# Kernel optimization log

Measured on AMD Instinct MI355X. Metric: run time of the kernel, lower is better.

Reference implementation:

```python
import jax, jax.numpy as jnp
import numpy as np

N_NODES = 50000
N_EDGES = 300000
HID = 256


def setup_inputs() -> dict:
    key = jax.random.key(0)
    ks = jax.random.split(key, 8)
    s = lambda fan_in: 1.0 / np.sqrt(fan_in)
    return {
        "node_embeddings": jax.random.normal(ks[0], (N_NODES, HID), dtype=jnp.float32),
        "edge_index": jax.random.randint(ks[1], (2, N_EDGES), 0, N_NODES, dtype=jnp.int64),
        "edge_attr": jax.random.normal(ks[2], (N_EDGES, 3), dtype=jnp.float32),
        "W1": jax.random.normal(ks[3], (2 * HID + 3, HID), dtype=jnp.float32) * s(2 * HID + 3),
        "b1": jnp.zeros((HID,), dtype=jnp.float32),
        "W2": jax.random.normal(ks[4], (HID, HID // 2), dtype=jnp.float32) * s(HID),
        "b2": jnp.zeros((HID // 2,), dtype=jnp.float32),
        "W3": jax.random.normal(ks[5], (HID // 2, HID // 4), dtype=jnp.float32) * s(HID // 2),
        "b3": jnp.zeros((HID // 4,), dtype=jnp.float32),
        "W4": jax.random.normal(ks[6], (HID // 4, 3), dtype=jnp.float32) * s(HID // 4),
        "b4": jnp.zeros((3,), dtype=jnp.float32),
    }


def reference(node_embeddings, edge_index, edge_attr, W1, b1, W2, b2, W3, b3, W4, b4):
    # Gather source/target node embeddings: [E, H] each
    src = node_embeddings[edge_index[0]]
    dst = node_embeddings[edge_index[1]]
    feats = jnp.concatenate([src, dst, edge_attr], axis=-1)  # [E, 2H+3]
    # edge_encoder: Linear -> ReLU -> (Dropout=identity in eval) -> Linear
    h = jax.nn.relu(feats @ W1 + b1)
    h = h @ W2 + b2  # [E, H//2]
    # classifier: Linear -> ReLU -> Linear
    h = jax.nn.relu(h @ W3 + b3)
    logits = h @ W4 + b4  # [E, 3]
    return logits
```

## Files before the change

kernel.cpp:

```cpp
#include <hip/hip_runtime.h>
#include <hip/hip_bf16.h>
#include <stdint.h>
#include <stddef.h>


#define NN 50000
#define NE 300000
#define KG(kq,g2) ((kq)*2+(g2))

using bf16x8 = __attribute__((ext_vector_type(8))) short;
using f32x16 = __attribute__((ext_vector_type(16))) float;
using f32x4  = __attribute__((ext_vector_type(4))) float;
using f32x2  = __attribute__((ext_vector_type(2))) float;
using u32x4  = __attribute__((ext_vector_type(4))) unsigned int;
using u32x2  = __attribute__((ext_vector_type(2))) unsigned int;

#define OFF_PQ   0ULL
#define SZ_PQ    (50000ULL*512ULL*2ULL)
#define OFF_W1   (OFF_PQ + SZ_PQ)
#define SZ_W1    (512ULL*256ULL*2ULL)
#define OFF_W1C  (OFF_W1 + SZ_W1)
#define SZ_W1C   (3ULL*256ULL*4ULL)
#define OFF_W2   (OFF_W1C + SZ_W1C)
#define SZ_W2    (128ULL*256ULL*2ULL)
#define OFF_W3   (OFF_W2 + SZ_W2)
#define SZ_W3    (64ULL*128ULL*2ULL)
#define OFF_W4   (OFF_W3 + SZ_W3)
#define SZ_W4    (16ULL*64ULL*2ULL)
#define OFF_FLAG (OFF_W4 + SZ_W4)
#define WS_NEED  (OFF_FLAG + 16ULL)

__device__ __forceinline__ unsigned short f2bf(float x){
  unsigned u = __float_as_uint(x);
  unsigned r = 0x7FFFu + ((u >> 16) & 1u);
  return (unsigned short)((u + r) >> 16);
}
__device__ __forceinline__ unsigned cvtpk(float lo, float hi){
  unsigned r;
  asm("v_cvt_pk_bf16_f32 %0, %1, %2" : "=v"(r) : "v"(lo), "v"(hi));
  return r;
}
__device__ __forceinline__ f32x2 unpk(unsigned w){
  f32x2 r;
  r[0] = __uint_as_float(w << 16);
  r[1] = __uint_as_float(w & 0xFFFF0000u);
  return r;
}
__device__ __forceinline__ f32x16 mfma32(bf16x8 a, bf16x8 b, f32x16 c){
  return __builtin_amdgcn_mfma_f32_32x32x16_bf16(a, b, c, 0, 0, 0);
}
__device__ __forceinline__ f32x4 mfma16(bf16x8 a, bf16x8 b, f32x4 c){
  return __builtin_amdgcn_mfma_f32_16x16x32_bf16(a, b, c, 0, 0, 0);
}
__device__ __forceinline__ f32x16 zero16(){
  f32x16 v;
#pragma unroll
  for (int i = 0; i < 16; ++i) v[i] = 0.f;
  return v;
}

__global__ void prep_pack(const float* __restrict__ W1, const float* __restrict__ W2,
                          const float* __restrict__ W3, const float* __restrict__ W4,
                          const int* __restrict__ ei32, char* __restrict__ ws)
{
  int i = blockIdx.x * 256 + threadIdx.x;
  unsigned short* w1i = (unsigned short*)(ws + OFF_W1);
  unsigned short* w2i = (unsigned short*)(ws + OFF_W2);
  unsigned short* w3i = (unsigned short*)(ws + OFF_W3);
  unsigned short* w4i = (unsigned short*)(ws + OFF_W4);

  if (i < 131072){
    int j = i & 7, out = (i >> 3) & 511, kg = i >> 12;
    int k = (kg >> 1)*16 + (kg & 1)*8 + j;
    float v = (out < 256) ? W1[(size_t)k*256 + out]
                          : W1[(size_t)(256 + k)*256 + (out - 256)];
    w1i[i] = f2bf(v);
  } else if (i < 131072 + 32768){
    int i2 = i - 131072;
    int j = i2 & 7, out = (i2 >> 3) & 127, sg = i2 >> 10;
    int k = (sg >> 2)*32 + (sg & 3)*8 + j;
    w2i[i2] = f2bf(W2[(size_t)k*128 + out]);
  } else if (i < 131072 + 32768 + 8192){
    int i3 = i - 131072 - 32768;
    int j = i3 & 7, out = (i3 >> 3) & 63, sg = i3 >> 9;
    int k = (sg >> 2)*32 + (sg & 3)*8 + j;
    w3i[i3] = f2bf(W3[(size_t)k*64 + out]);
  } else if (i < 131072 + 32768 + 8192 + 1024){
    int i4 = i - 131072 - 32768 - 8192;
    int j = i4 & 7, out = (i4 >> 3) & 15, sg = i4 >> 7;
    int k = (sg >> 2)*32 + (sg & 3)*8 + j;
    w4i[i4] = (out < 3) ? f2bf(W4[(size_t)k*3 + out]) : (unsigned short)0;
  }
  if (i < 768){
    float* w1c = (float*)(ws + OFF_W1C);
    w1c[i] = W1[(size_t)(512 + i/256)*256 + (i & 255)];
  }
  if (i == 0){
    int f = 1;
    for (int t = 1; t < 64; t += 2) if (ei32[t] != 0) { f = 0; break; }
    *(int*)(ws + OFF_FLAG) = f;
  }
}

__global__ __launch_bounds__(512, 4) void gemm1(const float* __restrict__ emb,
                                                const float* __restrict__ b1,
                                                char* __restrict__ ws)
{
  __shared__ __align__(16) unsigned short embL[32*64*8];

  const int tid = threadIdx.x;
  const int wv = tid >> 6, l = tid & 63, ln = l & 31, g2 = l >> 5;
  const int bid = blockIdx.x;
  const int nb = (bid >> 1) * 64;
  const int oh = bid & 1;
  const int ob = oh*256 + wv*32;
  const unsigned short* w1L = (const unsigned short*)(ws + OFF_W1);
  unsigned short* PQ = (unsigned short*)(ws + OFF_PQ);

  bf16x8 aw[16];
#pragma unroll
  for (int kq = 0; kq < 16; ++kq)
    aw[kq] = *(const bf16x8*)(w1L + ((size_t)KG(kq,g2)*512 + ob + ln)*8);

#pragma unroll
  for (int it = 0; it < 8; ++it){
    int u = it*512 + tid;
    int kg = u >> 7, node = (u >> 1) & 63, half = u & 1;
    int n = nb + node; if (n >= NN) n = NN - 1;
    int k = (kg >> 1)*16 + (kg & 1)*8 + half*4;
    f32x4 e = *(const f32x4*)(emb + (size_t)n*256 + k);
    u32x2 w; w[0] = cvtpk(e[0], e[1]); w[1] = cvtpk(e[2], e[3]);
    *(u32x2*)(embL + (size_t)kg*512 + node*8 + half*4) = w;
  }
  __syncthreads();

  f32x16 acc0 = zero16(), acc1 = zero16();
#pragma unroll
  for (int kq = 0; kq < 16; ++kq){
    bf16x8 b0  = *(const bf16x8*)(embL + ((size_t)KG(kq,g2)*64 +      ln)*8);
    bf16x8 b1v = *(const bf16x8*)(embL + ((size_t)KG(kq,g2)*64 + 32 + ln)*8);
    acc0 = mfma32(aw[kq], b0,  acc0);
    acc1 = mfma32(aw[kq], b1v, acc1);
  }

#pragma unroll
  for (int bg = 0; bg < 2; ++bg){
    int n = nb + bg*32 + ln;
    if (n < NN){
#pragma unroll
      for (int rr = 0; rr < 4; ++rr){
        int o = ob + rr*8 + g2*4;
        f32x4 bv = {0.f,0.f,0.f,0.f};
        if (oh == 0) bv = *(const f32x4*)(b1 + o);
        unsigned d0, d1;
        if (bg == 0){
          d0 = cvtpk(acc0[rr*4+0]+bv[0], acc0[rr*4+1]+bv[1]);
          d1 = cvtpk(acc0[rr*4+2]+bv[2], acc0[rr*4+3]+bv[3]);
        } else {
          d0 = cvtpk(acc1[rr*4+0]+bv[0], acc1[rr*4+1]+bv[1]);
          d1 = cvtpk(acc1[rr*4+2]+bv[2], acc1[rr*4+3]+bv[3]);
        }
        u32x2 st = {d0, d1};
        *(u32x2*)(PQ + (size_t)n*512 + o) = st;
      }
    }
  }
}


#define PAIRX(LO, HI, D) ((D)==0 ? (f32x2){(LO)[0],(LO)[1]} : \
                          (D)==1 ? (f32x2){(LO)[2],(LO)[3]} : \
                          (D)==2 ? (f32x2){(HI)[0],(HI)[1]} : \
                                   (f32x2){(HI)[2],(HI)[3]})

#define L2STEP(S, PC, QC)                                                      \
  {                                                                            \
    const int ks_ = (S);                                                       \
    const int kb = ks_*32 + g4*8;                                              \
    f32x4 w0lo = *(const f32x4*)(w1c_lds +   0 + kb);                          \
    f32x4 w0hi = *(const f32x4*)(w1c_lds +   4 + kb);                          \
    f32x4 w1lo = *(const f32x4*)(w1c_lds + 256 + kb);                          \
    f32x4 w1hi = *(const f32x4*)(w1c_lds + 260 + kb);                          \
    f32x4 w2lo = *(const f32x4*)(w1c_lds + 512 + kb);                          \
    f32x4 w2hi = *(const f32x4*)(w1c_lds + 516 + kb);                          \
    u32x4 pu = __builtin_bit_cast(u32x4, PC);                                  \
    u32x4 qu = __builtin_bit_cast(u32x4, QC);                                  \
    f32x2 z2 = {0.f, 0.f};                                                     \
    unsigned bu0, bu1, bu2, bu3;                                               \
    _Pragma("unroll")                                                          \
    for (int d = 0; d < 4; ++d){                                               \
      f32x2 h = unpk(pu[d]) + unpk(qu[d]);                                     \
      h += PAIRX(w0lo, w0hi, d) * at0;                                         \
      h += PAIRX(w1lo, w1hi, d) * at1;                                         \
      h += PAIRX(w2lo, w2hi, d) * at2;                                         \
      h = __builtin_elementwise_max(h, z2);                                    \
      unsigned c = cvtpk(h[0], h[1]);                                          \
      if (d==0) bu0 = c; else if (d==1) bu1 = c; else if (d==2) bu2 = c;       \
      else bu3 = c;                                                            \
    }                                                                          \
    u32x4 buv = {bu0, bu1, bu2, bu3};                                          \
    bf16x8 b = __builtin_bit_cast(bf16x8, buv);                                \
    const char* abase = smem + (size_t)(ks_*4 + g4)*2048 + c16*16;             \
    _Pragma("unroll")                                                          \
    for (int t = 0; t < 8; ++t){                                               \
      bf16x8 af = *(const bf16x8*)(abase + t*256);                             \
      acc2[t] = mfma16(af, b, acc2[t]);                                        \
    }                                                                          \
  }

__global__ __launch_bounds__(512, 4) void fused(const int* __restrict__ eidx,
                                                const float* __restrict__ attr,
                                                const float* __restrict__ b2,
                                                const float* __restrict__ b3,
                                                const float* __restrict__ b4,
                                                const char* __restrict__ ws,
                                                float* __restrict__ out)
{
  __shared__ __align__(16) char smem[68608];
  const int tid = threadIdx.x;
  const int wv = tid >> 6, l = tid & 63, c16 = l & 15, g4 = l >> 4;

  const unsigned short* PQ = (const unsigned short*)(ws + OFF_PQ);
  const float* W1c = (const float*)(ws + OFF_W1C);
  const int flag64 = *(const int*)(ws + OFF_FLAG);
  const float* w1c_lds = (const float*)(smem + 65536);

  const int eb = blockIdx.x * 128 + wv * 16;
  const int e = eb + c16;
  const bool ev = (e < NE);
  const int ec = ev ? e : 0;
  const int si = flag64 ? eidx[2*(size_t)ec]        : eidx[ec];
  const int di = flag64 ? eidx[2*((size_t)NE + ec)] : eidx[NE + ec];

  const unsigned short* Prow = PQ + (size_t)si*512 + g4*8;
  const unsigned short* Qrow = PQ + (size_t)di*512 + 256 + g4*8;
  bf16x8 p0 = *(const bf16x8*)(Prow +   0), p1 = *(const bf16x8*)(Prow +  32);
  bf16x8 p2 = *(const bf16x8*)(Prow +  64), p3 = *(const bf16x8*)(Prow +  96);
  bf16x8 p4 = *(const bf16x8*)(Prow + 128), p5 = *(const bf16x8*)(Prow + 160);
  bf16x8 p6 = *(const bf16x8*)(Prow + 192), p7 = *(const bf16x8*)(Prow + 224);
  bf16x8 q0 = *(const bf16x8*)(Qrow +   0), q1 = *(const bf16x8*)(Qrow +  32);
  bf16x8 q2 = *(const bf16x8*)(Qrow +  64), q3 = *(const bf16x8*)(Qrow +  96);
  bf16x8 q4 = *(const bf16x8*)(Qrow + 128), q5 = *(const bf16x8*)(Qrow + 160);
  bf16x8 q6 = *(const bf16x8*)(Qrow + 192), q7 = *(const bf16x8*)(Qrow + 224);

  const float at0 = ev ? attr[(size_t)ec*3 + 0] : 0.f;
  const float at1 = ev ? attr[(size_t)ec*3 + 1] : 0.f;
  const float at2 = ev ? attr[(size_t)ec*3 + 2] : 0.f;

  {
    const uint4* src = (const uint4*)(ws + OFF_W2);
    uint4* dst = (uint4*)smem;
#pragma unroll
    for (int it = 0; it < 8; ++it) dst[it*512 + tid] = src[it*512 + tid];
    if (tid < 192) ((f32x4*)(smem + 65536))[tid] = ((const f32x4*)W1c)[tid];
  }
  __syncthreads();

  f32x4 acc2[8];
#pragma unroll
  for (int t = 0; t < 8; ++t) acc2[t] = (f32x4){0.f,0.f,0.f,0.f};

  L2STEP(0, p0, q0);
  L2STEP(1, p1, q1);
  L2STEP(2, p2, q2);
  L2STEP(3, p3, q3);
  L2STEP(4, p4, q4);
  L2STEP(5, p5, q5);
  L2STEP(6, p6, q6);
  L2STEP(7, p7, q7);

  __syncthreads();

  {
    const uint4* s3 = (const uint4*)(ws + OFF_W3);
    uint4* d3 = (uint4*)(smem + 36864);
    for (int i = tid; i < 1152; i += 512) d3[i] = s3[i];
  }

  unsigned short* hslot = (unsigned short*)(smem + wv*4352);
#pragma unroll
  for (int t = 0; t < 8; ++t){
    f32x4 bv = *(const f32x4*)(b2 + t*16 + g4*4);
    unsigned d0 = cvtpk(acc2[t][0]+bv[0], acc2[t][1]+bv[1]);
    unsigned d1 = cvtpk(acc2[t][2]+bv[2], acc2[t][3]+bv[3]);
    u32x2 st = {d0, d1};
    *(u32x2*)(hslot + (size_t)c16*136 + t*16 + g4*4) = st;
  }
  __syncthreads();

  f32x4 acc3[4];
#pragma unroll
  for (int t = 0; t < 4; ++t) acc3[t] = (f32x4){0.f,0.f,0.f,0.f};
  const char* w3b = smem + 36864;
#pragma unroll
  for (int ks = 0; ks < 4; ++ks){
    bf16x8 bb = *(const bf16x8*)(hslot + (size_t)c16*136 + ks*32 + g4*8);
    const char* ab = w3b + (size_t)(ks*4 + g4)*1024 + c16*16;
#pragma unroll
    for (int t = 0; t < 4; ++t){
      bf16x8 af = *(const bf16x8*)(ab + t*256);
      acc3[t] = mfma16(af, bb, acc3[t]);
    }
  }

#pragma unroll
  for (int t = 0; t < 4; ++t){
    f32x4 bv = *(const f32x4*)(b3 + t*16 + g4*4);
    unsigned d0 = cvtpk(fmaxf(acc3[t][0]+bv[0],0.f), fmaxf(acc3[t][1]+bv[1],0.f));
    unsigned d1 = cvtpk(fmaxf(acc3[t][2]+bv[2],0.f), fmaxf(acc3[t][3]+bv[3],0.f));
    u32x2 st = {d0, d1};
    *(u32x2*)(hslot + (size_t)c16*136 + t*16 + g4*4) = st;
  }

  f32x4 acc4 = {0.f,0.f,0.f,0.f};
  const char* w4b = smem + 53248;
#pragma unroll
  for (int ks = 0; ks < 2; ++ks){
    bf16x8 bb = *(const bf16x8*)(hslot + (size_t)c16*136 + ks*32 + g4*8);
    bf16x8 af = *(const bf16x8*)(w4b + (size_t)(ks*4 + g4)*256 + c16*16);
    acc4 = mfma16(af, bb, acc4);
  }
  if (g4 == 0 && ev){
    out[(size_t)e*3 + 0] = acc4[0] + b4[0];
    out[(size_t)e*3 + 1] = acc4[1] + b4[1];
    out[(size_t)e*3 + 2] = acc4[2] + b4[2];
  }
}

extern "C" void kernel_launch(void* const* d_in, const int* in_sizes, int n_in,
                              void* d_out, int out_size, void* d_ws, size_t ws_size,
                              hipStream_t stream)
{
  const float* emb  = (const float*)d_in[0];
  const int*   eidx = (const int*)  d_in[1];
  const float* attr = (const float*)d_in[2];
  const float* W1   = (const float*)d_in[3];
  const float* b1   = (const float*)d_in[4];
  const float* W2   = (const float*)d_in[5];
  const float* b2   = (const float*)d_in[6];
  const float* W3   = (const float*)d_in[7];
  const float* b3   = (const float*)d_in[8];
  const float* W4   = (const float*)d_in[9];
  const float* b4   = (const float*)d_in[10];
  char* ws = (char*)d_ws;
  float* out = (float*)d_out;

  if (ws_size < WS_NEED) return;

  prep_pack<<<676, 256, 0, stream>>>(W1, W2, W3, W4, eidx, ws);
  gemm1<<<((NN + 63)/64)*2, 512, 0, stream>>>(emb, b1, ws);
  fused<<<(NE + 127)/128, 512, 0, stream>>>(eidx, attr, b2, b3, b4, ws, out);
}
```

Baseline: 121.8 us.

## Stream layer weights from global, shrink fused blocks, and restage gemm1 output through LDS

The fused edge kernel no longer copies W2/W3/W4 and the attr weights into shared memory behind block-wide barriers. Each wave now reads those weight fragments straight from global/L2 and keeps only small per-wave LDS slots for the hidden activations. P/Q rows are loaded four at a time with rolling prefetch to cut register pressure, and blocks shrink to 256 threads of 64 edges. gemm1 now has each wave compute 64 output columns over two 64-node tiles per block, staging results in LDS so the PQ rows are written as coalesced 16-byte stores. The cost is repeated global weight reads per wave and more registers and barriers in gemm1.

```diff
diff --git a/kernel.cpp b/kernel.cpp
--- a/kernel.cpp
+++ b/kernel.cpp
@@ -102,68 +102,90 @@
   }
 }
 
-__global__ __launch_bounds__(512, 4) void gemm1(const float* __restrict__ emb,
+__global__ __launch_bounds__(512, 2) void gemm1(const float* __restrict__ emb,
                                                 const float* __restrict__ b1,
                                                 char* __restrict__ ws)
 {
-  __shared__ __align__(16) unsigned short embL[32*64*8];
+  __shared__ __align__(16) unsigned short U[16896];
 
   const int tid = threadIdx.x;
   const int wv = tid >> 6, l = tid & 63, ln = l & 31, g2 = l >> 5;
-  const int bid = blockIdx.x;
-  const int nb = (bid >> 1) * 64;
-  const int oh = bid & 1;
-  const int ob = oh*256 + wv*32;
+  const int ob = wv * 64;
   const unsigned short* w1L = (const unsigned short*)(ws + OFF_W1);
   unsigned short* PQ = (unsigned short*)(ws + OFF_PQ);
 
-  bf16x8 aw[16];
-#pragma unroll
-  for (int kq = 0; kq < 16; ++kq)
-    aw[kq] = *(const bf16x8*)(w1L + ((size_t)KG(kq,g2)*512 + ob + ln)*8);
-
-#pragma unroll
-  for (int it = 0; it < 8; ++it){
-    int u = it*512 + tid;
-    int kg = u >> 7, node = (u >> 1) & 63, half = u & 1;
-    int n = nb + node; if (n >= NN) n = NN - 1;
-    int k = (kg >> 1)*16 + (kg & 1)*8 + half*4;
-    f32x4 e = *(const f32x4*)(emb + (size_t)n*256 + k);
-    u32x2 w; w[0] = cvtpk(e[0], e[1]); w[1] = cvtpk(e[2], e[3]);
-    *(u32x2*)(embL + (size_t)kg*512 + node*8 + half*4) = w;
-  }
-  __syncthreads();
-
-  f32x16 acc0 = zero16(), acc1 = zero16();
+  bf16x8 aw[2][16];
 #pragma unroll
   for (int kq = 0; kq < 16; ++kq){
-    bf16x8 b0  = *(const bf16x8*)(embL + ((size_t)KG(kq,g2)*64 +      ln)*8);
-    bf16x8 b1v = *(const bf16x8*)(embL + ((size_t)KG(kq,g2)*64 + 32 + ln)*8);
-    acc0 = mfma32(aw[kq], b0,  acc0);
-    acc1 = mfma32(aw[kq], b1v, acc1);
-  }
-
-#pragma unroll
-  for (int bg = 0; bg < 2; ++bg){
-    int n = nb + bg*32 + ln;
-    if (n < NN){
-#pragma unroll
-      for (int rr = 0; rr < 4; ++rr){
-        int o = ob + rr*8 + g2*4;
-        f32x4 bv = {0.f,0.f,0.f,0.f};
-        if (oh == 0) bv = *(const f32x4*)(b1 + o);
-        unsigned d0, d1;
-        if (bg == 0){
-          d0 = cvtpk(acc0[rr*4+0]+bv[0], acc0[rr*4+1]+bv[1]);
-          d1 = cvtpk(acc0[rr*4+2]+bv[2], acc0[rr*4+3]+bv[3]);
-        } else {
-          d0 = cvtpk(acc1[rr*4+0]+bv[0], acc1[rr*4+1]+bv[1]);
-          d1 = cvtpk(acc1[rr*4+2]+bv[2], acc1[rr*4+3]+bv[3]);
-        }
-        u32x2 st = {d0, d1};
-        *(u32x2*)(PQ + (size_t)n*512 + o) = st;
-      }
+#pragma unroll
+    for (int t2 = 0; t2 < 2; ++t2)
+      aw[t2][kq] = *(const bf16x8*)(w1L + ((size_t)KG(kq,g2)*512 + ob + t2*32 + ln)*8);
+  }
+
+#pragma unroll 1
+  for (int rep = 0; rep < 2; ++rep){
+    const int nb = (blockIdx.x*2 + rep) * 64;
+    __syncthreads();
+
+#pragma unroll
+    for (int it = 0; it < 8; ++it){
+      int u = it*512 + tid;
+      int kg = u >> 7, node = (u >> 1) & 63, half = u & 1;
+      int n = nb + node; if (n >= NN) n = NN - 1;
+      int k = (kg >> 1)*16 + (kg & 1)*8 + half*4;
+      f32x4 e = *(const f32x4*)(emb + (size_t)n*256 + k);
+      u32x2 w; w[0] = cvtpk(e[0], e[1]); w[1] = cvtpk(e[2], e[3]);
+      *(u32x2*)(U + (size_t)kg*512 + node*8 + half*4) = w;
     }
+    __syncthreads();
+
+    f32x16 acc[2][2];
+    acc[0][0] = zero16(); acc[0][1] = zero16();
+    acc[1][0] = zero16(); acc[1][1] = zero16();
+#pragma unroll
+    for (int kq = 0; kq < 16; ++kq){
+      bf16x8 b0  = *(const bf16x8*)(U + ((size_t)KG(kq,g2)*64 +      ln)*8);
+      bf16x8 b1v = *(const bf16x8*)(U + ((size_t)KG(kq,g2)*64 + 32 + ln)*8);
+      acc[0][0] = mfma32(aw[0][kq], b0,  acc[0][0]);
+      acc[1][0] = mfma32(aw[1][kq], b0,  acc[1][0]);
+      acc[0][1] = mfma32(aw[0][kq], b1v, acc[0][1]);
+      acc[1][1] = mfma32(aw[1][kq], b1v, acc[1][1]);
+    }
+    __syncthreads();
+
+    const int r_ = tid >> 4;
+    const int j_ = tid & 15;
+#define G1PASS(BG)                                                             \
+    {                                                                          \
+      _Pragma("unroll")                                                        \
+      for (int t2 = 0; t2 < 2; ++t2){                                          \
+        _Pragma("unroll")                                                      \
+        for (int rr = 0; rr < 4; ++rr){                                        \
+          int o = ob + t2*32 + rr*8 + g2*4;                                    \
+          f32x4 bv = {0.f,0.f,0.f,0.f};                                        \
+          if (ob + t2*32 < 256) bv = *(const f32x4*)(b1 + o);                  \
+          unsigned d0 = cvtpk(acc[t2][BG][rr*4+0]+bv[0], acc[t2][BG][rr*4+1]+bv[1]); \
+          unsigned d1 = cvtpk(acc[t2][BG][rr*4+2]+bv[2], acc[t2][BG][rr*4+3]+bv[3]); \
+          u32x2 st = {d0, d1};                                                 \
+          *(u32x2*)(U + (size_t)ln*516 + o) = st;                              \
+        }                                                                      \
+      }                                                                        \
+      __syncthreads();                                                         \
+      {                                                                        \
+        int n = nb + (BG)*32 + r_;                                             \
+        if (n < NN){                                                           \
+          _Pragma("unroll")                                                    \
+          for (int ii = 0; ii < 4; ++ii){                                      \
+            uint4 v = *(const uint4*)(U + (size_t)r_*516 + ii*128 + j_*8);     \
+            *(uint4*)(PQ + (size_t)n*512 + ii*128 + j_*8) = v;                 \
+          }                                                                    \
+        }                                                                      \
+      }                                                                        \
+    }
+    G1PASS(0);
+    __syncthreads();
+    G1PASS(1);
+#undef G1PASS
   }
 }
 
@@ -173,16 +195,15 @@
                           (D)==2 ? (f32x2){(HI)[0],(HI)[1]} : \
                                    (f32x2){(HI)[2],(HI)[3]})
 
-#define L2STEP(S, PC, QC)                                                      \
+#define L2G(S, PC, QC)                                                         \
   {                                                                            \
-    const int ks_ = (S);                                                       \
-    const int kb = ks_*32 + g4*8;                                              \
-    f32x4 w0lo = *(const f32x4*)(w1c_lds +   0 + kb);                          \
-    f32x4 w0hi = *(const f32x4*)(w1c_lds +   4 + kb);                          \
-    f32x4 w1lo = *(const f32x4*)(w1c_lds + 256 + kb);                          \
-    f32x4 w1hi = *(const f32x4*)(w1c_lds + 260 + kb);                          \
-    f32x4 w2lo = *(const f32x4*)(w1c_lds + 512 + kb);                          \
-    f32x4 w2hi = *(const f32x4*)(w1c_lds + 516 + kb);                          \
+    const int kb = (S)*32 + g4*8;                                              \
+    f32x4 w0lo = *(const f32x4*)(w1cg +   0 + kb);                             \
+    f32x4 w0hi = *(const f32x4*)(w1cg +   4 + kb);                             \
+    f32x4 w1lo = *(const f32x4*)(w1cg + 256 + kb);                             \
+    f32x4 w1hi = *(const f32x4*)(w1cg + 260 + kb);                             \
+    f32x4 w2lo = *(const f32x4*)(w1cg + 512 + kb);                             \
+    f32x4 w2hi = *(const f32x4*)(w1cg + 516 + kb);                             \
     u32x4 pu = __builtin_bit_cast(u32x4, PC);                                  \
     u32x4 qu = __builtin_bit_cast(u32x4, QC);                                  \
     f32x2 z2 = {0.f, 0.f};                                                     \
@@ -200,15 +221,19 @@
     }                                                                          \
     u32x4 buv = {bu0, bu1, bu2, bu3};                                          \
     bf16x8 b = __builtin_bit_cast(bf16x8, buv);                                \
-    const char* abase = smem + (size_t)(ks_*4 + g4)*2048 + c16*16;             \
+    if ((S) + 4 <= 7){                                                         \
+      PC = *(const bf16x8*)(Prow + ((S)+4)*32);                                \
+      QC = *(const bf16x8*)(Qrow + ((S)+4)*32);                                \
+    }                                                                          \
+    const unsigned short* ab = w2g + ((size_t)((S)*4 + g4)*128 + c16)*8;       \
     _Pragma("unroll")                                                          \
     for (int t = 0; t < 8; ++t){                                               \
-      bf16x8 af = *(const bf16x8*)(abase + t*256);                             \
+      bf16x8 af = *(const bf16x8*)(ab + t*128);                                \
       acc2[t] = mfma16(af, b, acc2[t]);                                        \
     }                                                                          \
   }
 
-__global__ __launch_bounds__(512, 4) void fused(const int* __restrict__ eidx,
+__global__ __launch_bounds__(256, 4) void fused(const int* __restrict__ eidx,
                                                 const float* __restrict__ attr,
                                                 const float* __restrict__ b2,
                                                 const float* __restrict__ b3,
@@ -216,89 +241,70 @@
                                                 const char* __restrict__ ws,
                                                 float* __restrict__ out)
 {
-  __shared__ __align__(16) char smem[68608];
+  __shared__ __align__(16) unsigned short h2s[4][16*136];
+  __shared__ __align__(16) unsigned short h3s[4][16*72];
+
   const int tid = threadIdx.x;
   const int wv = tid >> 6, l = tid & 63, c16 = l & 15, g4 = l >> 4;
-
-  const unsigned short* PQ = (const unsigned short*)(ws + OFF_PQ);
-  const float* W1c = (const float*)(ws + OFF_W1C);
+  unsigned short* h2w = h2s[wv];
+  unsigned short* h3w = h3s[wv];
+
+  const unsigned short* PQ  = (const unsigned short*)(ws + OFF_PQ);
+  const unsigned short* w2g = (const unsigned short*)(ws + OFF_W2);
+  const unsigned short* w3g = (const unsigned short*)(ws + OFF_W3);
+  const unsigned short* w4g = (const unsigned short*)(ws + OFF_W4);
+  const float* w1cg = (const float*)(ws + OFF_W1C);
   const int flag64 = *(const int*)(ws + OFF_FLAG);
-  const float* w1c_lds = (const float*)(smem + 65536);
-
-  const int eb = blockIdx.x * 128 + wv * 16;
-  const int e = eb + c16;
+
+  const int e = blockIdx.x * 64 + wv * 16 + c16;
   const bool ev = (e < NE);
   const int ec = ev ? e : 0;
   const int si = flag64 ? eidx[2*(size_t)ec]        : eidx[ec];
   const int di = flag64 ? eidx[2*((size_t)NE + ec)] : eidx[NE + ec];
-
-  const unsigned short* Prow = PQ + (size_t)si*512 + g4*8;
-  const unsigned short* Qrow = PQ + (size_t)di*512 + 256 + g4*8;
-  bf16x8 p0 = *(const bf16x8*)(Prow +   0), p1 = *(const bf16x8*)(Prow +  32);
-  bf16x8 p2 = *(const bf16x8*)(Prow +  64), p3 = *(const bf16x8*)(Prow +  96);
-  bf16x8 p4 = *(const bf16x8*)(Prow + 128), p5 = *(const bf16x8*)(Prow + 160);
-  bf16x8 p6 = *(const bf16x8*)(Prow + 192), p7 = *(const bf16x8*)(Prow + 224);
-  bf16x8 q0 = *(const bf16x8*)(Qrow +   0), q1 = *(const bf16x8*)(Qrow +  32);
-  bf16x8 q2 = *(const bf16x8*)(Qrow +  64), q3 = *(const bf16x8*)(Qrow +  96);
-  bf16x8 q4 = *(const bf16x8*)(Qrow + 128), q5 = *(const bf16x8*)(Qrow + 160);
-  bf16x8 q6 = *(const bf16x8*)(Qrow + 192), q7 = *(const bf16x8*)(Qrow + 224);
-
   const float at0 = ev ? attr[(size_t)ec*3 + 0] : 0.f;
   const float at1 = ev ? attr[(size_t)ec*3 + 1] : 0.f;
   const float at2 = ev ? attr[(size_t)ec*3 + 2] : 0.f;
 
-  {
-    const uint4* src = (const uint4*)(ws + OFF_W2);
-    uint4* dst = (uint4*)smem;
-#pragma unroll
-    for (int it = 0; it < 8; ++it) dst[it*512 + tid] = src[it*512 + tid];
-    if (tid < 192) ((f32x4*)(smem + 65536))[tid] = ((const f32x4*)W1c)[tid];
-  }
-  __syncthreads();
+  const unsigned short* Prow = PQ + (size_t)si*512 + g4*8;
+  const unsigned short* Qrow = PQ + (size_t)di*512 + 256 + g4*8;
+
+  bf16x8 pA = *(const bf16x8*)(Prow +  0), qA = *(const bf16x8*)(Qrow +  0);
+  bf16x8 pB = *(const bf16x8*)(Prow + 32), qB = *(const bf16x8*)(Qrow + 32);
+  bf16x8 pC = *(const bf16x8*)(Prow + 64), qC = *(const bf16x8*)(Qrow + 64);
+  bf16x8 pD = *(const bf16x8*)(Prow + 96), qD = *(const bf16x8*)(Qrow + 96);
 
   f32x4 acc2[8];
 #pragma unroll
   for (int t = 0; t < 8; ++t) acc2[t] = (f32x4){0.f,0.f,0.f,0.f};
 
-  L2STEP(0, p0, q0);
-  L2STEP(1, p1, q1);
-  L2STEP(2, p2, q2);
-  L2STEP(3, p3, q3);
-  L2STEP(4, p4, q4);
-  L2STEP(5, p5, q5);
-  L2STEP(6, p6, q6);
-  L2STEP(7, p7, q7);
-
-  __syncthreads();
-
-  {
-    const uint4* s3 = (const uint4*)(ws + OFF_W3);
-    uint4* d3 = (uint4*)(smem + 36864);
-    for (int i = tid; i < 1152; i += 512) d3[i] = s3[i];
-  }
-
-  unsigned short* hslot = (unsigned short*)(smem + wv*4352);
+  L2G(0, pA, qA);
+  L2G(1, pB, qB);
+  L2G(2, pC, qC);
+  L2G(3, pD, qD);
+  L2G(4, pA, qA);
+  L2G(5, pB, qB);
+  L2G(6, pC, qC);
+  L2G(7, pD, qD);
+
 #pragma unroll
   for (int t = 0; t < 8; ++t){
     f32x4 bv = *(const f32x4*)(b2 + t*16 + g4*4);
     unsigned d0 = cvtpk(acc2[t][0]+bv[0], acc2[t][1]+bv[1]);
     unsigned d1 = cvtpk(acc2[t][2]+bv[2], acc2[t][3]+bv[3]);
     u32x2 st = {d0, d1};
-    *(u32x2*)(hslot + (size_t)c16*136 + t*16 + g4*4) = st;
-  }
-  __syncthreads();
+    *(u32x2*)(h2w + (size_t)c16*136 + t*16 + g4*4) = st;
+  }
 
   f32x4 acc3[4];
 #pragma unroll
   for (int t = 0; t < 4; ++t) acc3[t] = (f32x4){0.f,0.f,0.f,0.f};
-  const char* w3b = smem + 36864;
 #pragma unroll
   for (int ks = 0; ks < 4; ++ks){
-    bf16x8 bb = *(const bf16x8*)(hslot + (size_t)c16*136 + ks*32 + g4*8);
-    const char* ab = w3b + (size_t)(ks*4 + g4)*1024 + c16*16;
+    bf16x8 bb = *(const bf16x8*)(h2w + (size_t)c16*136 + ks*32 + g4*8);
+    const unsigned short* ab3 = w3g + ((size_t)(ks*4 + g4)*64 + c16)*8;
 #pragma unroll
     for (int t = 0; t < 4; ++t){
-      bf16x8 af = *(const bf16x8*)(ab + t*256);
+      bf16x8 af = *(const bf16x8*)(ab3 + t*128);
       acc3[t] = mfma16(af, bb, acc3[t]);
     }
   }
@@ -309,15 +315,14 @@
     unsigned d0 = cvtpk(fmaxf(acc3[t][0]+bv[0],0.f), fmaxf(acc3[t][1]+bv[1],0.f));
     unsigned d1 = cvtpk(fmaxf(acc3[t][2]+bv[2],0.f), fmaxf(acc3[t][3]+bv[3],0.f));
     u32x2 st = {d0, d1};
-    *(u32x2*)(hslot + (size_t)c16*136 + t*16 + g4*4) = st;
+    *(u32x2*)(h3w + (size_t)c16*72 + t*16 + g4*4) = st;
   }
 
   f32x4 acc4 = {0.f,0.f,0.f,0.f};
-  const char* w4b = smem + 53248;
 #pragma unroll
   for (int ks = 0; ks < 2; ++ks){
-    bf16x8 bb = *(const bf16x8*)(hslot + (size_t)c16*136 + ks*32 + g4*8);
-    bf16x8 af = *(const bf16x8*)(w4b + (size_t)(ks*4 + g4)*256 + c16*16);
+    bf16x8 af = *(const bf16x8*)(w4g + ((size_t)(ks*4 + g4)*16 + c16)*8);
+    bf16x8 bb = *(const bf16x8*)(h3w + (size_t)c16*72 + ks*32 + g4*8);
     acc4 = mfma16(af, bb, acc4);
   }
   if (g4 == 0 && ev){
@@ -348,6 +353,6 @@
   if (ws_size < WS_NEED) return;
 
   prep_pack<<<676, 256, 0, stream>>>(W1, W2, W3, W4, eidx, ws);
-  gemm1<<<((NN + 63)/64)*2, 512, 0, stream>>>(emb, b1, ws);
-  fused<<<(NE + 127)/128, 512, 0, stream>>>(eidx, attr, b2, b3, b4, ws, out);
-}
+  gemm1<<<(NN + 127)/128, 512, 0, stream>>>(emb, b1, ws);
+  fused<<<(NE + 63)/64, 256, 0, stream>>>(eidx, attr, b2, b3, b4, ws, out);
+}
```

Result: slower. 160.6 us (+31.9%).
